# Performance work log

Hardware: AMD Instinct MI355X
Metric: run time of the kernel (lower is better)

The kernel has to match this reference:

```python
import jax, jax.numpy as jnp
import numpy as np

EPS = 1e-5  # torch.nn.LayerNorm default
NUM_HEADS = 8


def _layernorm(x, g, b):
    mu = jnp.mean(x, axis=-1, keepdims=True)
    var = jnp.mean((x - mu) ** 2, axis=-1, keepdims=True)
    return (x - mu) * jax.lax.rsqrt(var + EPS) * g + b


def setup_inputs() -> dict:
    key = jax.random.key(0)
    ks = jax.random.split(key, 8)
    B, S, D = 4, 2048, 512
    scale = 0.02
    return {
        'x': jax.random.normal(ks[0], (B, S, D), dtype=jnp.float32),
        'gene_types': jax.random.randint(ks[1], (B, S), 0, 2),
        'tf_g': jnp.ones((D,), jnp.float32), 'tf_b': jnp.zeros((D,), jnp.float32),
        'tg_g': jnp.ones((D,), jnp.float32), 'tg_b': jnp.zeros((D,), jnp.float32),
        'in_proj_w': jax.random.normal(ks[2], (3 * D, D), dtype=jnp.float32) * scale,
        'in_proj_b': jnp.zeros((3 * D,), jnp.float32),
        'out_proj_w': jax.random.normal(ks[3], (D, D), dtype=jnp.float32) * scale,
        'out_proj_b': jnp.zeros((D,), jnp.float32),
        'w1': jax.random.normal(ks[4], (D // 2, D), dtype=jnp.float32) * scale,
        'b1': jnp.zeros((D // 2,), jnp.float32),
        'w2': jax.random.normal(ks[5], (1, D // 2), dtype=jnp.float32) * scale,
        'b2': jnp.zeros((1,), jnp.float32),
    }


def reference(x, gene_types, tf_g, tf_b, tg_g, tg_b,
              in_proj_w, in_proj_b, out_proj_w, out_proj_b,
              w1, b1, w2, b2):
    B, S, D = x.shape
    H = NUM_HEADS
    HD = D // H
    # --- vectorized per-token conditional LayerNorm (gene_type 0 -> tf, 1 -> target, else passthrough) ---
    gt = gene_types[..., None]
    xn = jnp.where(gt == 0, _layernorm(x, tf_g, tf_b),
                   jnp.where(gt == 1, _layernorm(x, tg_g, tg_b), x))
    # --- multi-head self-attention (torch MultiheadAttention, batch_first) ---
    qkv = xn @ in_proj_w.T + in_proj_b            # [B,S,3D]
    q, k, v = jnp.split(qkv, 3, axis=-1)
    to_heads = lambda t: t.reshape(B, S, H, HD).transpose(0, 2, 1, 3)  # [B,H,S,HD]
    q, k, v = to_heads(q), to_heads(k), to_heads(v)
    scores = jnp.einsum('bhqd,bhkd->bhqk', q, k) / jnp.sqrt(jnp.float32(HD))
    attn = jax.nn.softmax(scores, axis=-1)
    o = jnp.einsum('bhqk,bhkd->bhqd', attn, v)
    o = o.transpose(0, 2, 1, 3).reshape(B, S, D)
    o = o @ out_proj_w.T + out_proj_b
    xr = xn + o                                    # residual
    # --- regulatory strength gate: Linear -> SiLU -> Linear -> Sigmoid ---
    h = jax.nn.silu(xr @ w1.T + b1)                # [B,S,D/2]
    strength = jax.nn.sigmoid(h @ w2.T + b2)       # [B,S,1]
    return xr * strength
```

## Files before the change

kernel.cpp:

```cpp
#include <hip/hip_runtime.h>

typedef __bf16 bf16;
typedef __bf16 bf16x4_t __attribute__((ext_vector_type(4)));
typedef __bf16 bf16x8_t __attribute__((ext_vector_type(8)));
typedef float f32x4_t __attribute__((ext_vector_type(4)));

#define MFMA16(a, b, c) __builtin_amdgcn_mfma_f32_16x16x32_bf16(a, b, c, 0, 0, 0)

__global__ __launch_bounds__(256) void castln_k(const float* __restrict__ Wqkv,
                                                const float* __restrict__ Wout,
                                                const float* __restrict__ W1,
                                                bf16* __restrict__ wq,
                                                bf16* __restrict__ wo,
                                                bf16* __restrict__ w1b,
                                                const float* __restrict__ x,
                                                const int* __restrict__ gt,
                                                const float* __restrict__ tfg,
                                                const float* __restrict__ tfb,
                                                const float* __restrict__ tgg,
                                                const float* __restrict__ tgb,
                                                bf16* __restrict__ xn) {
    if (blockIdx.x < 4608) {
        int i = blockIdx.x * 256 + threadIdx.x;
        if (i < 786432) wq[i] = (bf16)Wqkv[i];
        else if (i < 1048576) wo[i - 786432] = (bf16)Wout[i - 786432];
        else if (i < 1179648) w1b[i - 1048576] = (bf16)W1[i - 1048576];
        return;
    }
    int wid = threadIdx.x >> 6, lane = threadIdx.x & 63;
    int t = (blockIdx.x - 4608) * 4 + wid;
    const float4* xr = (const float4*)(x + (size_t)t * 512);
    float4 a = xr[lane * 2], b = xr[lane * 2 + 1];
    float s = (a.x + a.y) + (a.z + a.w) + (b.x + b.y) + (b.z + b.w);
    float sq = a.x * a.x + a.y * a.y + a.z * a.z + a.w * a.w +
               b.x * b.x + b.y * b.y + b.z * b.z + b.w * b.w;
    for (int m = 1; m < 64; m <<= 1) {
        s += __shfl_xor(s, m, 64);
        sq += __shfl_xor(sq, m, 64);
    }
    float mean = s * (1.f / 512.f);
    float var = fmaxf(sq * (1.f / 512.f) - mean * mean, 0.f);
    float rstd = rsqrtf(var + 1e-5f);
    int g = gt[t];
    float4 o0, o1;
    if (g < 2) {
        const float4* gp = (const float4*)(g ? tgg : tfg);
        const float4* bp = (const float4*)(g ? tgb : tfb);
        float4 g0 = gp[lane * 2], g1 = gp[lane * 2 + 1];
        float4 b0 = bp[lane * 2], b1 = bp[lane * 2 + 1];
        o0.x = (a.x - mean) * rstd * g0.x + b0.x;
        o0.y = (a.y - mean) * rstd * g0.y + b0.y;
        o0.z = (a.z - mean) * rstd * g0.z + b0.z;
        o0.w = (a.w - mean) * rstd * g0.w + b0.w;
        o1.x = (b.x - mean) * rstd * g1.x + b1.x;
        o1.y = (b.y - mean) * rstd * g1.y + b1.y;
        o1.z = (b.z - mean) * rstd * g1.z + b1.z;
        o1.w = (b.w - mean) * rstd * g1.w + b1.w;
    } else {
        o0 = a; o1 = b;
    }
    bf16* xo = xn + (size_t)t * 512 + lane * 8;
    bf16x4_t p0, p1;
    p0[0] = (bf16)o0.x; p0[1] = (bf16)o0.y; p0[2] = (bf16)o0.z; p0[3] = (bf16)o0.w;
    p1[0] = (bf16)o1.x; p1[1] = (bf16)o1.y; p1[2] = (bf16)o1.z; p1[3] = (bf16)o1.w;
    *(bf16x4_t*)xo = p0;
    *(bf16x4_t*)(xo + 4) = p1;
}

__global__ __launch_bounds__(256) void gemmqkv_k(const bf16* __restrict__ A,
                                                 const bf16* __restrict__ B,
                                                 const float* __restrict__ bias,
                                                 bf16* __restrict__ q,
                                                 bf16* __restrict__ kk,
                                                 bf16* __restrict__ vt) {
    int m0 = blockIdx.x * 128, n0 = blockIdx.y * 128;
    int tid = threadIdx.x;
    int lane = tid & 63, w = tid >> 6;
    int quad = lane >> 4, l15 = lane & 15;
    int wm = (w >> 1) * 64, wn = (w & 1) * 64;
    __shared__ bf16 smem[128 * 144];
    bf16* As = smem;
    bf16* Bs = smem + 128 * 72;
    f32x4_t acc[4][4] = {};
    int srow = tid >> 3, ssub = tid & 7;
    const bf16* Ab = A + (size_t)(m0 + srow) * 512 + ssub * 8;
    const bf16* Bb = B + (size_t)(n0 + srow) * 512 + ssub * 8;
    uint4 pa[4], pb[4];
    auto gload = [&](int s) {
        int k0 = s * 64;
#pragma unroll
        for (int i = 0; i < 4; ++i) {
            pa[i] = *(const uint4*)(Ab + (size_t)(i * 32) * 512 + k0);
            pb[i] = *(const uint4*)(Bb + (size_t)(i * 32) * 512 + k0);
        }
    };
    auto sstore = [&]() {
#pragma unroll
        for (int i = 0; i < 4; ++i) {
            *(uint4*)&As[(i * 32 + srow) * 72 + ssub * 8] = pa[i];
            *(uint4*)&Bs[(i * 32 + srow) * 72 + ssub * 8] = pb[i];
        }
    };
    gload(0);
    sstore();
    for (int s = 0; s < 8; ++s) {
        __syncthreads();
        if (s < 7) gload(s + 1);
#pragma unroll
        for (int ks = 0; ks < 2; ++ks) {
            bf16x8_t af[4], bfr[4];
            int koff = ks * 32 + quad * 8;
#pragma unroll
            for (int mt = 0; mt < 4; ++mt)
                af[mt] = *(const bf16x8_t*)&As[(wm + mt * 16 + l15) * 72 + koff];
#pragma unroll
            for (int nt = 0; nt < 4; ++nt)
                bfr[nt] = *(const bf16x8_t*)&Bs[(wn + nt * 16 + l15) * 72 + koff];
#pragma unroll
            for (int mt = 0; mt < 4; ++mt)
#pragma unroll
                for (int nt = 0; nt < 4; ++nt)
                    acc[mt][nt] = MFMA16(af[mt], bfr[nt], acc[mt][nt]);
        }
        __syncthreads();
        if (s < 7) sstore();
    }
    if (blockIdx.y < 8) {
#pragma unroll
        for (int mt = 0; mt < 4; ++mt) {
#pragma unroll
            for (int nt = 0; nt < 4; ++nt) {
                int gcol = n0 + wn + nt * 16 + l15;
                float bcol = bias[gcol];
#pragma unroll
                for (int r = 0; r < 4; ++r) {
                    int grow = m0 + wm + mt * 16 + quad * 4 + r;
                    float v = acc[mt][nt][r] + bcol;
                    int d = gcol & 511;
                    int hh = d >> 6, hd = d & 63;
                    int b = grow >> 11, ssi = grow & 2047;
                    size_t idx = (((size_t)(b * 8 + hh)) * 2048 + ssi) * 64 + hd;
                    if (gcol < 512) q[idx] = (bf16)(v * 0.180336880111f);
                    else kk[idx] = (bf16)v;
                }
            }
        }
    } else {
        __syncthreads();
#pragma unroll
        for (int mt = 0; mt < 4; ++mt)
#pragma unroll
            for (int nt = 0; nt < 4; ++nt) {
                int gcol = n0 + wn + nt * 16 + l15;
                float bcol = bias[gcol];
#pragma unroll
                for (int r = 0; r < 4; ++r) {
                    int tok = wm + mt * 16 + quad * 4 + r;
                    smem[tok * 136 + wn + nt * 16 + l15] = (bf16)(acc[mt][nt][r] + bcol);
                }
            }
        __syncthreads();
        int dl = tid >> 1, seg = tid & 1;
        int d = (n0 - 1024) + dl;
        int hh = d >> 6, hd = d & 63;
        int b = m0 >> 11, ssi0 = m0 & 2047;
        bf16* dst = vt + ((size_t)(b * 8 + hh) * 64 + hd) * 2048 + ssi0 + seg * 64;
#pragma unroll
        for (int u = 0; u < 8; ++u) {
            bf16 tmp[8];
#pragma unroll
            for (int j = 0; j < 8; ++j) tmp[j] = smem[(seg * 64 + u * 8 + j) * 136 + dl];
            *(uint4*)(dst + u * 8) = *(uint4*)tmp;
        }
    }
}

__global__ __launch_bounds__(256) void attn_k(const bf16* __restrict__ q,
                                              const bf16* __restrict__ k,
                                              const bf16* __restrict__ vt,
                                              bf16* __restrict__ pO,
                                              float* __restrict__ pL) {
    int bh = blockIdx.y;
    int q0 = blockIdx.x * 64;
    int sz = blockIdx.z;
    int tid = threadIdx.x;
    int lane = tid & 63, w = tid >> 6;
    int quad = lane >> 4, l15 = lane & 15;
    __shared__ bf16 Ks[64 * 72];
    __shared__ bf16 Vs[64 * 72];
    __shared__ bf16 Ps[64 * 72];
    const bf16* qb = q + (size_t)bh * 2048 * 64;
    const bf16* kb = k + (size_t)bh * 2048 * 64;
    const bf16* vb = vt + (size_t)bh * 64 * 2048;
    bf16x8_t qf[2];
#pragma unroll
    for (int ks = 0; ks < 2; ++ks)
        qf[ks] = *(const bf16x8_t*)(qb + (size_t)(q0 + w * 16 + l15) * 64 + ks * 32 + quad * 8);
    bf16x8_t ones8;
#pragma unroll
    for (int i = 0; i < 8; ++i) ones8[i] = (bf16)1.0f;
    f32x4_t oacc[4] = {};
    f32x4_t lacc = {};
    int srow = tid >> 3, ssub = tid & 7;
    for (int kt = sz * 8; kt < sz * 8 + 8; ++kt) {
        int kbase = kt * 64;
        __syncthreads();
#pragma unroll
        for (int i = 0; i < 2; ++i) {
            int row = i * 32 + srow;
            *(uint4*)&Ks[row * 72 + ssub * 8] = *(const uint4*)(kb + (size_t)(kbase + row) * 64 + ssub * 8);
            *(uint4*)&Vs[row * 72 + ssub * 8] = *(const uint4*)(vb + (size_t)row * 2048 + kbase + ssub * 8);
        }
        __syncthreads();
        f32x4_t sacc[4] = {};
#pragma unroll
        for (int ks = 0; ks < 2; ++ks) {
            bf16x8_t kf[4];
            int koff = ks * 32 + quad * 8;
#pragma unroll
            for (int nt = 0; nt < 4; ++nt) kf[nt] = *(const bf16x8_t*)&Ks[(nt * 16 + l15) * 72 + koff];
#pragma unroll
            for (int nt = 0; nt < 4; ++nt)
                sacc[nt] = MFMA16(qf[ks], kf[nt], sacc[nt]);
        }
#pragma unroll
        for (int nt = 0; nt < 4; ++nt)
#pragma unroll
            for (int r = 0; r < 4; ++r)
                Ps[(w * 16 + quad * 4 + r) * 72 + nt * 16 + l15] = (bf16)exp2f(sacc[nt][r]);
#pragma unroll
        for (int ks = 0; ks < 2; ++ks) {
            int koff = ks * 32 + quad * 8;
            bf16x8_t pf, vf[4];
            pf = *(const bf16x8_t*)&Ps[(w * 16 + l15) * 72 + koff];
#pragma unroll
            for (int nt = 0; nt < 4; ++nt) vf[nt] = *(const bf16x8_t*)&Vs[(nt * 16 + l15) * 72 + koff];
#pragma unroll
            for (int nt = 0; nt < 4; ++nt)
                oacc[nt] = MFMA16(pf, vf[nt], oacc[nt]);
            lacc = MFMA16(pf, ones8, lacc);
        }
    }
    size_t obase = ((size_t)(sz * 32 + bh) * 2048 + q0);
#pragma unroll
    for (int r = 0; r < 4; ++r) {
        int row = w * 16 + quad * 4 + r;
#pragma unroll
        for (int nt = 0; nt < 4; ++nt)
            pO[(obase + row) * 64 + nt * 16 + l15] = (bf16)oacc[nt][r];
        if (l15 == 0) pL[obase + row] = lacc[r];
    }
}

__global__ __launch_bounds__(256) void gemmo_k(const bf16* __restrict__ pO,
                                               const float* __restrict__ pL,
                                               const bf16* __restrict__ B,
                                               const float* __restrict__ bias,
                                               const bf16* __restrict__ xn,
                                               float* __restrict__ xrf) {
    int m0 = blockIdx.x * 128, n0 = blockIdx.y * 128;
    int tid = threadIdx.x;
    int lane = tid & 63, w = tid >> 6;
    int quad = lane >> 4, l15 = lane & 15;
    int wm = (w >> 1) * 64, wn = (w & 1) * 64;
    __shared__ bf16 As[128 * 72];
    __shared__ bf16 Bs[128 * 72];
    f32x4_t acc[4][4] = {};
    int srow = tid >> 3, ssub = tid & 7;
    const bf16* Bb = B + (size_t)(n0 + srow) * 512 + ssub * 8;
    bf16x8_t pa[4];
    uint4 pb[4];
    auto gload = [&](int s) {
        int k0 = s * 64;
#pragma unroll
        for (int i = 0; i < 4; ++i) {
            int t = m0 + i * 32 + srow;
            int b = t >> 11, ssi = t & 2047;
            float lsum = 0.f;
            float facc[8] = {};
#pragma unroll
            for (int sp = 0; sp < 4; ++sp) {
                size_t r = ((size_t)(sp * 32 + b * 8 + s)) * 2048 + ssi;
                lsum += pL[r];
                bf16x8_t av = *(const bf16x8_t*)(pO + r * 64 + ssub * 8);
#pragma unroll
                for (int j = 0; j < 8; ++j) facc[j] += (float)av[j];
            }
            float inv = 1.f / lsum;
            bf16x8_t c;
#pragma unroll
            for (int j = 0; j < 8; ++j) c[j] = (bf16)(facc[j] * inv);
            pa[i] = c;
            pb[i] = *(const uint4*)(Bb + (size_t)(i * 32) * 512 + k0);
        }
    };
    auto sstore = [&]() {
#pragma unroll
        for (int i = 0; i < 4; ++i) {
            *(bf16x8_t*)&As[(i * 32 + srow) * 72 + ssub * 8] = pa[i];
            *(uint4*)&Bs[(i * 32 + srow) * 72 + ssub * 8] = pb[i];
        }
    };
    gload(0);
    sstore();
    for (int s = 0; s < 8; ++s) {
        __syncthreads();
        if (s < 7) gload(s + 1);
#pragma unroll
        for (int ks = 0; ks < 2; ++ks) {
            bf16x8_t af[4], bfr[4];
            int koff = ks * 32 + quad * 8;
#pragma unroll
            for (int mt = 0; mt < 4; ++mt)
                af[mt] = *(const bf16x8_t*)&As[(wm + mt * 16 + l15) * 72 + koff];
#pragma unroll
            for (int nt = 0; nt < 4; ++nt)
                bfr[nt] = *(const bf16x8_t*)&Bs[(wn + nt * 16 + l15) * 72 + koff];
#pragma unroll
            for (int mt = 0; mt < 4; ++mt)
#pragma unroll
                for (int nt = 0; nt < 4; ++nt)
                    acc[mt][nt] = MFMA16(af[mt], bfr[nt], acc[mt][nt]);
        }
        __syncthreads();
        if (s < 7) sstore();
    }
#pragma unroll
    for (int mt = 0; mt < 4; ++mt) {
#pragma unroll
        for (int nt = 0; nt < 4; ++nt) {
            int gcol = n0 + wn + nt * 16 + l15;
            float bcol = bias[gcol];
#pragma unroll
            for (int r = 0; r < 4; ++r) {
                int grow = m0 + wm + mt * 16 + quad * 4 + r;
                size_t idx = (size_t)grow * 512 + gcol;
                xrf[idx] = acc[mt][nt][r] + bcol + (float)xn[idx];
            }
        }
    }
}

__global__ __launch_bounds__(256) void mlp_k(const bf16* __restrict__ B,
                                             const float* __restrict__ b1,
                                             const float* __restrict__ w2,
                                             const float* __restrict__ b2,
                                             const float* __restrict__ xrf,
                                             float* __restrict__ out) {
    int m0 = blockIdx.x * 32;
    int tid = threadIdx.x;
    int lane = tid & 63, w = tid >> 6;
    int quad = lane >> 4, l15 = lane & 15;
    int wn = w * 64;
    __shared__ bf16 As[32 * 72];
    __shared__ bf16 Bs[256 * 72];
    __shared__ float red[4][32];
    __shared__ float st[32];
    f32x4_t acc[2][4] = {};
    int srow = tid >> 3, ssub = tid & 7;
    bf16x8_t pa;
    uint4 pb[8];
    auto gload = [&](int s) {
        int k0 = s * 64;
        const float* ar = xrf + (size_t)(m0 + srow) * 512 + ssub * 8 + k0;
        float4 f0 = *(const float4*)ar;
        float4 f1 = *(const float4*)(ar + 4);
        pa[0] = (bf16)f0.x; pa[1] = (bf16)f0.y; pa[2] = (bf16)f0.z; pa[3] = (bf16)f0.w;
        pa[4] = (bf16)f1.x; pa[5] = (bf16)f1.y; pa[6] = (bf16)f1.z; pa[7] = (bf16)f1.w;
#pragma unroll
        for (int i = 0; i < 8; ++i)
            pb[i] = *(const uint4*)(B + (size_t)(i * 32 + srow) * 512 + ssub * 8 + k0);
    };
    auto sstore = [&]() {
        *(bf16x8_t*)&As[srow * 72 + ssub * 8] = pa;
#pragma unroll
        for (int i = 0; i < 8; ++i)
            *(uint4*)&Bs[(i * 32 + srow) * 72 + ssub * 8] = pb[i];
    };
    gload(0);
    sstore();
    for (int s = 0; s < 8; ++s) {
        __syncthreads();
        if (s < 7) gload(s + 1);
#pragma unroll
        for (int ks = 0; ks < 2; ++ks) {
            int koff = ks * 32 + quad * 8;
            bf16x8_t af[2], bfr[4];
#pragma unroll
            for (int mt = 0; mt < 2; ++mt)
                af[mt] = *(const bf16x8_t*)&As[(mt * 16 + l15) * 72 + koff];
#pragma unroll
            for (int nt = 0; nt < 4; ++nt)
                bfr[nt] = *(const bf16x8_t*)&Bs[(wn + nt * 16 + l15) * 72 + koff];
#pragma unroll
            for (int mt = 0; mt < 2; ++mt)
#pragma unroll
                for (int nt = 0; nt < 4; ++nt)
                    acc[mt][nt] = MFMA16(af[mt], bfr[nt], acc[mt][nt]);
        }
        __syncthreads();
        if (s < 7) sstore();
    }
    f32x4_t ds[2] = {};
#pragma unroll
    for (int mt = 0; mt < 2; ++mt)
#pragma unroll
        for (int nt = 0; nt < 4; ++nt) {
            int gcol = wn + nt * 16 + l15;
            float bb = b1[gcol], ww = w2[gcol];
#pragma unroll
            for (int r = 0; r < 4; ++r) {
                float v = acc[mt][nt][r] + bb;
                float sv = v / (1.f + __expf(-v));
                ds[mt][r] += sv * ww;
            }
        }
#pragma unroll
    for (int m = 1; m < 16; m <<= 1)
#pragma unroll
        for (int mt = 0; mt < 2; ++mt)
#pragma unroll
            for (int r = 0; r < 4; ++r) ds[mt][r] += __shfl_xor(ds[mt][r], m, 64);
    if (l15 == 0) {
#pragma unroll
        for (int mt = 0; mt < 2; ++mt)
#pragma unroll
            for (int r = 0; r < 4; ++r) red[w][mt * 16 + quad * 4 + r] = ds[mt][r];
    }
    __syncthreads();
    if (tid < 32) {
        float d = red[0][tid] + red[1][tid] + red[2][tid] + red[3][tid] + b2[0];
        st[tid] = 1.f / (1.f + __expf(-d));
    }
    __syncthreads();
    int row = tid >> 3, seg = tid & 7;
    float sr = st[row];
    const float4* x4 = (const float4*)(xrf + (size_t)(m0 + row) * 512);
    float4* o4 = (float4*)(out + (size_t)(m0 + row) * 512);
#pragma unroll
    for (int jj = 0; jj < 16; ++jj) {
        float4 xv = x4[jj * 8 + seg];
        float4 ov;
        ov.x = xv.x * sr; ov.y = xv.y * sr; ov.z = xv.z * sr; ov.w = xv.w * sr;
        o4[jj * 8 + seg] = ov;
    }
}

extern "C" void kernel_launch(void* const* d_in, const int* in_sizes, int n_in,
                              void* d_out, int out_size, void* d_ws, size_t ws_size,
                              hipStream_t stream) {
    const float* x    = (const float*)d_in[0];
    const int*   gt   = (const int*)d_in[1];
    const float* tfg  = (const float*)d_in[2];
    const float* tfb  = (const float*)d_in[3];
    const float* tgg  = (const float*)d_in[4];
    const float* tgb  = (const float*)d_in[5];
    const float* Wqkv = (const float*)d_in[6];
    const float* bqkv = (const float*)d_in[7];
    const float* Wout = (const float*)d_in[8];
    const float* bout = (const float*)d_in[9];
    const float* W1   = (const float*)d_in[10];
    const float* b1   = (const float*)d_in[11];
    const float* w2   = (const float*)d_in[12];
    const float* b2   = (const float*)d_in[13];
    float* out = (float*)d_out;
    char* ws = (char*)d_ws;

    const size_t MB = 1024 * 1024;
    bf16*  wq  = (bf16*)(ws + 0);
    bf16*  wo  = (bf16*)(ws + 1536 * 512 * 2);
    bf16*  w1b = (bf16*)(ws + (1536 + 512) * 512 * 2);
    float* pL  = (float*)(ws + 2304 * 512 * 2);
    bf16*  xn  = (bf16*)(ws + 4 * MB);
    bf16*  q   = (bf16*)(ws + 12 * MB);
    bf16*  kk  = (bf16*)(ws + 20 * MB);
    float* xrf = (float*)(ws + 12 * MB);
    bf16*  vt  = (bf16*)(ws + 28 * MB);
    bf16*  pO  = (bf16*)(ws + 36 * MB);

    castln_k<<<6656, 256, 0, stream>>>(Wqkv, Wout, W1, wq, wo, w1b,
                                       x, gt, tfg, tfb, tgg, tgb, xn);
    gemmqkv_k<<<dim3(64, 12), 256, 0, stream>>>(xn, wq, bqkv, q, kk, vt);
    attn_k<<<dim3(32, 32, 4), 256, 0, stream>>>(q, kk, vt, pO, pL);
    gemmo_k<<<dim3(64, 4), 256, 0, stream>>>(pO, pL, wo, bout, xn, xrf);
    mlp_k<<<256, 256, 0, stream>>>(w1b, b1, w2, b2, xrf, out);
    (void)in_sizes; (void)n_in; (void)out_size; (void)ws_size;
}
```

Baseline: 319.0 us.

## Enlarge attention query tile to 256 rows per block for K/V reuse

```diff
diff --git a/kernel.cpp b/kernel.cpp
--- a/kernel.cpp
+++ b/kernel.cpp
@@ -181,26 +181,28 @@
                                               bf16* __restrict__ pO,
                                               float* __restrict__ pL) {
     int bh = blockIdx.y;
-    int q0 = blockIdx.x * 64;
+    int q0 = blockIdx.x * 256;
     int sz = blockIdx.z;
     int tid = threadIdx.x;
     int lane = tid & 63, w = tid >> 6;
     int quad = lane >> 4, l15 = lane & 15;
     __shared__ bf16 Ks[64 * 72];
     __shared__ bf16 Vs[64 * 72];
-    __shared__ bf16 Ps[64 * 72];
+    __shared__ bf16 Ps[256 * 72];
     const bf16* qb = q + (size_t)bh * 2048 * 64;
     const bf16* kb = k + (size_t)bh * 2048 * 64;
     const bf16* vb = vt + (size_t)bh * 64 * 2048;
-    bf16x8_t qf[2];
-#pragma unroll
-    for (int ks = 0; ks < 2; ++ks)
-        qf[ks] = *(const bf16x8_t*)(qb + (size_t)(q0 + w * 16 + l15) * 64 + ks * 32 + quad * 8);
+    bf16x8_t qf[4][2];
+#pragma unroll
+    for (int mt = 0; mt < 4; ++mt)
+#pragma unroll
+        for (int ks = 0; ks < 2; ++ks)
+            qf[mt][ks] = *(const bf16x8_t*)(qb + (size_t)(q0 + w * 64 + mt * 16 + l15) * 64 + ks * 32 + quad * 8);
     bf16x8_t ones8;
 #pragma unroll
     for (int i = 0; i < 8; ++i) ones8[i] = (bf16)1.0f;
-    f32x4_t oacc[4] = {};
-    f32x4_t lacc = {};
+    f32x4_t oacc[4][4] = {};
+    f32x4_t lacc[4] = {};
     int srow = tid >> 3, ssub = tid & 7;
     for (int kt = sz * 8; kt < sz * 8 + 8; ++kt) {
         int kbase = kt * 64;
@@ -212,44 +214,52 @@
             *(uint4*)&Vs[row * 72 + ssub * 8] = *(const uint4*)(vb + (size_t)row * 2048 + kbase + ssub * 8);
         }
         __syncthreads();
-        f32x4_t sacc[4] = {};
-#pragma unroll
-        for (int ks = 0; ks < 2; ++ks) {
-            bf16x8_t kf[4];
-            int koff = ks * 32 + quad * 8;
-#pragma unroll
-            for (int nt = 0; nt < 4; ++nt) kf[nt] = *(const bf16x8_t*)&Ks[(nt * 16 + l15) * 72 + koff];
-#pragma unroll
-            for (int nt = 0; nt < 4; ++nt)
-                sacc[nt] = MFMA16(qf[ks], kf[nt], sacc[nt]);
-        }
-#pragma unroll
-        for (int nt = 0; nt < 4; ++nt)
-#pragma unroll
-            for (int r = 0; r < 4; ++r)
-                Ps[(w * 16 + quad * 4 + r) * 72 + nt * 16 + l15] = (bf16)exp2f(sacc[nt][r]);
+#pragma unroll
+        for (int nt = 0; nt < 4; ++nt) {
+            f32x4_t sacc[4] = {};
+#pragma unroll
+            for (int ks = 0; ks < 2; ++ks) {
+                bf16x8_t kf = *(const bf16x8_t*)&Ks[(nt * 16 + l15) * 72 + ks * 32 + quad * 8];
+#pragma unroll
+                for (int mt = 0; mt < 4; ++mt)
+                    sacc[mt] = MFMA16(qf[mt][ks], kf, sacc[mt]);
+            }
+#pragma unroll
+            for (int mt = 0; mt < 4; ++mt)
+#pragma unroll
+                for (int r = 0; r < 4; ++r)
+                    Ps[(w * 64 + mt * 16 + quad * 4 + r) * 72 + nt * 16 + l15] = (bf16)exp2f(sacc[mt][r]);
+        }
 #pragma unroll
         for (int ks = 0; ks < 2; ++ks) {
             int koff = ks * 32 + quad * 8;
-            bf16x8_t pf, vf[4];
-            pf = *(const bf16x8_t*)&Ps[(w * 16 + l15) * 72 + koff];
-#pragma unroll
-            for (int nt = 0; nt < 4; ++nt) vf[nt] = *(const bf16x8_t*)&Vs[(nt * 16 + l15) * 72 + koff];
+            bf16x8_t pf[4], vf[4];
+#pragma unroll
+            for (int mt = 0; mt < 4; ++mt)
+                pf[mt] = *(const bf16x8_t*)&Ps[(w * 64 + mt * 16 + l15) * 72 + koff];
 #pragma unroll
             for (int nt = 0; nt < 4; ++nt)
-                oacc[nt] = MFMA16(pf, vf[nt], oacc[nt]);
-            lacc = MFMA16(pf, ones8, lacc);
+                vf[nt] = *(const bf16x8_t*)&Vs[(nt * 16 + l15) * 72 + koff];
+#pragma unroll
+            for (int mt = 0; mt < 4; ++mt) {
+#pragma unroll
+                for (int nt = 0; nt < 4; ++nt)
+                    oacc[mt][nt] = MFMA16(pf[mt], vf[nt], oacc[mt][nt]);
+                lacc[mt] = MFMA16(pf[mt], ones8, lacc[mt]);
+            }
         }
     }
     size_t obase = ((size_t)(sz * 32 + bh) * 2048 + q0);
 #pragma unroll
-    for (int r = 0; r < 4; ++r) {
-        int row = w * 16 + quad * 4 + r;
-#pragma unroll
-        for (int nt = 0; nt < 4; ++nt)
-            pO[(obase + row) * 64 + nt * 16 + l15] = (bf16)oacc[nt][r];
-        if (l15 == 0) pL[obase + row] = lacc[r];
-    }
+    for (int mt = 0; mt < 4; ++mt)
+#pragma unroll
+        for (int r = 0; r < 4; ++r) {
+            int row = w * 64 + mt * 16 + quad * 4 + r;
+#pragma unroll
+            for (int nt = 0; nt < 4; ++nt)
+                pO[(obase + row) * 64 + nt * 16 + l15] = (bf16)oacc[mt][nt][r];
+            if (l15 == 0) pL[obase + row] = lacc[mt][r];
+        }
 }
 
 __global__ __launch_bounds__(256) void gemmo_k(const bf16* __restrict__ pO,
@@ -481,7 +491,7 @@
     castln_k<<<6656, 256, 0, stream>>>(Wqkv, Wout, W1, wq, wo, w1b,
                                        x, gt, tfg, tfb, tgg, tgb, xn);
     gemmqkv_k<<<dim3(64, 12), 256, 0, stream>>>(xn, wq, bqkv, q, kk, vt);
-    attn_k<<<dim3(32, 32, 4), 256, 0, stream>>>(q, kk, vt, pO, pL);
+    attn_k<<<dim3(8, 32, 4), 256, 0, stream>>>(q, kk, vt, pO, pL);
     gemmo_k<<<dim3(64, 4), 256, 0, stream>>>(pO, pL, wo, bout, xn, xrf);
     mlp_k<<<256, 256, 0, stream>>>(w1b, b1, w2, b2, xrf, out);
     (void)in_sizes; (void)n_in; (void)out_size; (void)ws_size;
```

Result: no change. 317.1 us (-0.6%).
